# Kernel tuning notes

Measured on AMD Instinct MI355X. Metric: run time of the kernel, lower is better.

The kernel has to match this reference:

```python
import jax, jax.numpy as jnp
import numpy as np

N_NODES = 50000
N_EDGES = 1600000
IN_F = 256
OUT_F = 128
ALPHA = 0.2  # LeakyReLU negative slope
EPS = 1e-9


def setup_inputs() -> dict:
    key = jax.random.key(0)
    k1, k2, k3, k4 = jax.random.split(key, 4)
    x = jax.random.normal(k1, (N_NODES, IN_F), dtype=jnp.float32)
    edge_index = jax.random.randint(k2, (2, N_EDGES), 0, N_NODES, dtype=jnp.int64)
    # xavier_uniform-ish scale for params
    W = jax.random.normal(k3, (IN_F, OUT_F), dtype=jnp.float32) * (1.414 / np.sqrt(IN_F + OUT_F))
    a = jax.random.normal(k4, (1, 2 * OUT_F), dtype=jnp.float32) * (1.414 / np.sqrt(1 + 2 * OUT_F))
    return {"x": x, "edge_index": edge_index, "W": W, "a": a}


def reference(x, edge_index, W, a):
    N = x.shape[0]
    F = W.shape[1]
    h = x @ W                                  # [N, F]
    src = edge_index[0]                        # row indices (aggregation target)
    dst = edge_index[1]                        # col indices (neighbor source)
    a_src = a[0, :F]                           # split a.mm(cat(h_src, h_dst).T)
    a_dst = a[0, F:]
    score = h[src] @ a_src + h[dst] @ a_dst    # [E]
    e = jnp.exp(-jax.nn.leaky_relu(score, negative_slope=ALPHA))  # [E]
    # e_rowsum = A @ ones : sum of edge values per row
    rowsum = jax.ops.segment_sum(e, src, num_segments=N)          # [N]
    # h_prime = A @ h : weighted neighbor aggregation per row
    agg = jax.ops.segment_sum(e[:, None] * h[dst], src, num_segments=N)  # [N, F]
    h_prime = agg / (rowsum[:, None] + EPS)
    return jax.nn.elu(h_prime)  # concat=True -> elu
```

## Files before the change

kernel.cpp:

```cpp
#include <hip/hip_runtime.h>
#include <hip/hip_bf16.h>
#include <math.h>

#define N_NODES 50000
#define N_EDGES 1600000
#define IN_F 256
#define OUT_F 128
#define ALPHA 0.2f
#define EPS 1e-9f

#define NPB 32
#define BINS 1563
#define SUBCAP 1536
#define MAXDEG 128

#define PTILE2 4096
#define PBLKS ((N_EDGES + PTILE2 - 1) / PTILE2)

#define GROWS 32
#define GBLKS ((N_NODES + GROWS - 1) / GROWS)
#define XPITCH 264

typedef __attribute__((ext_vector_type(8))) short short8v;
typedef __attribute__((ext_vector_type(4))) float f32x4;

__device__ __forceinline__ unsigned short bf16r(float f) {
  unsigned u = __float_as_uint(f);
  u = (u + 0x7FFFu + ((u >> 16) & 1u)) >> 16;
  return (unsigned short)u;
}

__device__ __forceinline__ unsigned pk2(float a, float b) {
  unsigned ua = (__float_as_uint(a) + 0x8000u) >> 16;
  unsigned ub = (__float_as_uint(b) + 0x8000u) & 0xFFFF0000u;
  return ua | ub;
}

__global__ __launch_bounds__(256) void wcvt_k(const float* __restrict__ W,
                                              unsigned short* __restrict__ Bf) {
  int fid = blockIdx.x * 256 + threadIdx.x;
  int lane = fid & 63;
  int ks = (fid >> 6) & 7;
  int cg = (fid >> 9) & 1;
  int wv = fid >> 10;
  int col = wv * 32 + cg * 16 + (lane & 15);
  int k0 = ks * 32 + (lane >> 4) * 8;
  unsigned short v[8];
#pragma unroll
  for (int j = 0; j < 8; ++j)
    v[j] = bf16r(W[(size_t)(k0 + j) * OUT_F + col]);
  *reinterpret_cast<short8v*>(&Bf[(size_t)fid * 8]) = *reinterpret_cast<short8v*>(v);
}

__device__ __forceinline__ int load_idx(const int* __restrict__ ei32, int isI64,
                                        long long pos) {
  if (isI64) return (int)(reinterpret_cast<const long long*>(ei32)[pos]);
  return ei32[pos];
}

union SMemU {
  struct {
    unsigned short xsb[GROWS][XPITCH];
    float s1p[GROWS], s2p[GROWS];
  } g;
  struct {
    int hist[BINS], cur[BINS], gbase[BINS];
    int sf64;
  } p;
};

__global__ __launch_bounds__(256) void fused_k(const float* __restrict__ x,
                                               const unsigned short* __restrict__ Bf,
                                               const float* __restrict__ a,
                                               unsigned short* __restrict__ hbs,
                                               float* __restrict__ s1,
                                               float* __restrict__ s2,
                                               const int* __restrict__ ei,
                                               unsigned* __restrict__ bins,
                                               int* __restrict__ bincur) {
  __shared__ SMemU sm;
  const int t = threadIdx.x;

  if (blockIdx.x < PBLKS) {
    if (t < 64) {
      int nz = 0;
#pragma unroll
      for (int j = 0; j < 4; ++j) nz |= ei[2 * (t + j * 64) + 1];
      unsigned long long any = __ballot(nz != 0);
      if (t == 0) sm.p.sf64 = (any == 0ull) ? 1 : 0;
    }
    for (int i = t; i < BINS; i += 256) sm.p.hist[i] = 0;
    __syncthreads();
    const int f64 = sm.p.sf64;
    const int base = blockIdx.x * PTILE2;
    unsigned rec[16];
#pragma unroll
    for (int j = 0; j < 16; ++j) {
      int e = base + j * 256 + t;
      if (e < N_EDGES) {
        unsigned s = (unsigned)load_idx(ei, f64, e);
        unsigned d = (unsigned)load_idx(ei, f64, (long long)N_EDGES + e);
        rec[j] = (s << 16) | d;
        atomicAdd(&sm.p.hist[s >> 5], 1);
      } else rec[j] = 0xFFFFFFFFu;
    }
    __syncthreads();
    for (int i = t; i < BINS; i += 256) {
      sm.p.gbase[i] = sm.p.hist[i] ? atomicAdd(&bincur[i], sm.p.hist[i]) : 0;
      sm.p.cur[i] = 0;
    }
    __syncthreads();
#pragma unroll
    for (int j = 0; j < 16; ++j) {
      if (rec[j] != 0xFFFFFFFFu) {
        int bb = rec[j] >> 21;
        int pos = atomicAdd(&sm.p.cur[bb], 1);
        int o = sm.p.gbase[bb] + pos;
        if (o < SUBCAP) bins[(size_t)bb * SUBCAP + o] = rec[j];
      }
    }
    return;
  }

  const int gbid = blockIdx.x - PBLKS;
  const int lane = t & 63;
  const int wv = t >> 6;
  const int row0 = gbid * GROWS;
  const int wcol0 = wv * 32;
  const int lrow = lane & 15;
  const int hi = lane >> 4;
  const int lk = hi * 8;

  if (t < GROWS) { sm.g.s1p[t] = 0.f; sm.g.s2p[t] = 0.f; }

#pragma unroll
  for (int it = 0; it < 8; ++it) {
    int f4 = it * 256 + t;
    int row = f4 >> 6;
    int c4 = (f4 & 63) * 4;
    int gr = row0 + row;
    if (gr >= N_NODES) gr = N_NODES - 1;
    float4 u = *reinterpret_cast<const float4*>(&x[(size_t)gr * IN_F + c4]);
    unsigned* p = reinterpret_cast<unsigned*>(&sm.g.xsb[row][c4]);
    p[0] = pk2(u.x, u.y);
    p[1] = pk2(u.z, u.w);
  }

  short8v b[2][8];
#pragma unroll
  for (int cg = 0; cg < 2; ++cg)
#pragma unroll
    for (int ks = 0; ks < 8; ++ks)
      b[cg][ks] = *reinterpret_cast<const short8v*>(
          &Bf[(size_t)(((wv * 2 + cg) * 8 + ks) * 64 + lane) * 8]);

  float4 a1v = *reinterpret_cast<const float4*>(&a[wcol0 + 4 * hi]);
  float4 a1w = *reinterpret_cast<const float4*>(&a[wcol0 + 16 + 4 * hi]);
  float4 a2v = *reinterpret_cast<const float4*>(&a[128 + wcol0 + 4 * hi]);
  float4 a2w = *reinterpret_cast<const float4*>(&a[128 + wcol0 + 16 + 4 * hi]);
  __syncthreads();

#pragma unroll
  for (int rg = 0; rg < GROWS / 16; ++rg) {
    short8v av[8];
#pragma unroll
    for (int ks = 0; ks < 8; ++ks)
      av[ks] = *reinterpret_cast<const short8v*>(&sm.g.xsb[rg * 16 + lrow][ks * 32 + lk]);
    f32x4 acc0 = {0.f, 0.f, 0.f, 0.f};
    f32x4 acc1 = {0.f, 0.f, 0.f, 0.f};
#pragma unroll
    for (int ks = 0; ks < 8; ++ks) {
      acc0 = __builtin_amdgcn_mfma_f32_16x16x32_bf16(b[0][ks], av[ks], acc0, 0, 0, 0);
      acc1 = __builtin_amdgcn_mfma_f32_16x16x32_bf16(b[1][ks], av[ks], acc1, 0, 0, 0);
    }
    int xrow = row0 + rg * 16 + lrow;
    if (xrow < N_NODES) {
      uint2 o0 = {pk2(acc0[0], acc0[1]), pk2(acc0[2], acc0[3])};
      uint2 o1 = {pk2(acc1[0], acc1[1]), pk2(acc1[2], acc1[3])};
      *reinterpret_cast<uint2*>(&hbs[(size_t)xrow * OUT_F + wcol0 + 4 * hi]) = o0;
      *reinterpret_cast<uint2*>(&hbs[(size_t)xrow * OUT_F + wcol0 + 16 + 4 * hi]) = o1;
    }
    float p1 = acc0[0] * a1v.x + acc0[1] * a1v.y + acc0[2] * a1v.z + acc0[3] * a1v.w
             + acc1[0] * a1w.x + acc1[1] * a1w.y + acc1[2] * a1w.z + acc1[3] * a1w.w;
    float p2 = acc0[0] * a2v.x + acc0[1] * a2v.y + acc0[2] * a2v.z + acc0[3] * a2v.w
             + acc1[0] * a2w.x + acc1[1] * a2w.y + acc1[2] * a2w.z + acc1[3] * a2w.w;
    p1 += __shfl_xor(p1, 16, 64);
    p2 += __shfl_xor(p2, 16, 64);
    p1 += __shfl_xor(p1, 32, 64);
    p2 += __shfl_xor(p2, 32, 64);
    if (hi == 0) {
      atomicAdd(&sm.g.s1p[rg * 16 + lrow], p1);
      atomicAdd(&sm.g.s2p[rg * 16 + lrow], p2);
    }
  }
  __syncthreads();
  if (t < GROWS) {
    int g = row0 + t;
    if (g < N_NODES) { s1[g] = sm.g.s1p[t]; s2[g] = sm.g.s2p[t]; }
  }
}

__global__ __launch_bounds__(512) void aggc_k(const unsigned* __restrict__ bins,
                                              const int* __restrict__ bincur,
                                              const float* __restrict__ s1,
                                              const float* __restrict__ s2,
                                              const unsigned* __restrict__ hb,
                                              float* __restrict__ out) {
  __shared__ unsigned short sorted[SUBCAP];
  __shared__ uint2 ebuf[8][MAXDEG];
  __shared__ int hist[NPB], cur[NPB], rowptr[NPB + 1];
  const int t = threadIdx.x;
  const int b = blockIdx.x;
  const int lo = b * NPB;
  const int n_b = min(bincur[b], SUBCAP);
  const unsigned* bp = bins + (size_t)b * SUBCAP;

  if (t < NPB) hist[t] = 0;
  __syncthreads();
  unsigned rec[3];
#pragma unroll
  for (int r = 0; r < 3; ++r) {
    int i = t + r * 512;
    rec[r] = 0xFFFFFFFFu;
    if (i < n_b) {
      rec[r] = bp[i];
      atomicAdd(&hist[(rec[r] >> 16) & (NPB - 1)], 1);
    }
  }
  __syncthreads();
  if (t < NPB) {
    int c = hist[t];
    int incl = c;
#pragma unroll
    for (int off = 1; off < NPB; off <<= 1) {
      int v = __shfl_up(incl, off, 64);
      if (t >= off) incl += v;
    }
    rowptr[t + 1] = incl;
    cur[t] = incl - c;
    if (t == 0) rowptr[0] = 0;
  }
  __syncthreads();
#pragma unroll
  for (int r = 0; r < 3; ++r) {
    if (rec[r] != 0xFFFFFFFFu) {
      int sl = (rec[r] >> 16) & (NPB - 1);
      int pos = atomicAdd(&cur[sl], 1);
      sorted[pos] = (unsigned short)(rec[r] & 0xFFFFu);
    }
  }
  __syncthreads();

  const int wv = t >> 6, lane = t & 63;
  for (int i = 0; i < 4; ++i) {
    int nl = wv * 4 + i;
    int g = lo + nl;
    if (g >= N_NODES) continue;
    int rp = rowptr[nl];
    int cn = min(rowptr[nl + 1] - rp, MAXDEG);
    float s1u = s1[g];
    float rsl = 0.f;
    for (int j = lane; j < cn; j += 64) {
      unsigned d = sorted[rp + j];
      float sc = s1u + s2[d];
      float w = __expf(-fmaxf(sc, ALPHA * sc));
      ebuf[wv][j] = make_uint2(d << 6, __float_as_uint(w));
      rsl += w;
    }
#pragma unroll
    for (int m = 32; m >= 1; m >>= 1) rsl += __shfl_xor(rsl, m, 64);
    float accx = 0.f, accy = 0.f;
    int j = 0;
    for (; j + 7 < cn; j += 8) {
      uint4 e0 = *reinterpret_cast<const uint4*>(&ebuf[wv][j]);
      uint4 e1 = *reinterpret_cast<const uint4*>(&ebuf[wv][j + 2]);
      uint4 e2 = *reinterpret_cast<const uint4*>(&ebuf[wv][j + 4]);
      uint4 e3 = *reinterpret_cast<const uint4*>(&ebuf[wv][j + 6]);
      unsigned v0 = hb[e0.x | lane];
      unsigned v1 = hb[e0.z | lane];
      unsigned v2 = hb[e1.x | lane];
      unsigned v3 = hb[e1.z | lane];
      unsigned v4 = hb[e2.x | lane];
      unsigned v5 = hb[e2.z | lane];
      unsigned v6 = hb[e3.x | lane];
      unsigned v7 = hb[e3.z | lane];
      float w0 = __uint_as_float(e0.y), w1 = __uint_as_float(e0.w);
      float w2 = __uint_as_float(e1.y), w3 = __uint_as_float(e1.w);
      float w4 = __uint_as_float(e2.y), w5 = __uint_as_float(e2.w);
      float w6 = __uint_as_float(e3.y), w7 = __uint_as_float(e3.w);
      accx = fmaf(w0, __uint_as_float(v0 << 16), accx);
      accy = fmaf(w0, __uint_as_float(v0 & 0xFFFF0000u), accy);
      accx = fmaf(w1, __uint_as_float(v1 << 16), accx);
      accy = fmaf(w1, __uint_as_float(v1 & 0xFFFF0000u), accy);
      accx = fmaf(w2, __uint_as_float(v2 << 16), accx);
      accy = fmaf(w2, __uint_as_float(v2 & 0xFFFF0000u), accy);
      accx = fmaf(w3, __uint_as_float(v3 << 16), accx);
      accy = fmaf(w3, __uint_as_float(v3 & 0xFFFF0000u), accy);
      accx = fmaf(w4, __uint_as_float(v4 << 16), accx);
      accy = fmaf(w4, __uint_as_float(v4 & 0xFFFF0000u), accy);
      accx = fmaf(w5, __uint_as_float(v5 << 16), accx);
      accy = fmaf(w5, __uint_as_float(v5 & 0xFFFF0000u), accy);
      accx = fmaf(w6, __uint_as_float(v6 << 16), accx);
      accy = fmaf(w6, __uint_as_float(v6 & 0xFFFF0000u), accy);
      accx = fmaf(w7, __uint_as_float(v7 << 16), accx);
      accy = fmaf(w7, __uint_as_float(v7 & 0xFFFF0000u), accy);
    }
    for (; j < cn; ++j) {
      uint2 e = ebuf[wv][j];
      unsigned v0 = hb[e.x | lane];
      float w0 = __uint_as_float(e.y);
      accx = fmaf(w0, __uint_as_float(v0 << 16), accx);
      accy = fmaf(w0, __uint_as_float(v0 & 0xFFFF0000u), accy);
    }
    float inv = 1.0f / (rsl + EPS);
    float px = accx * inv, py = accy * inv;
    px = px > 0.f ? px : expm1f(px);
    py = py > 0.f ? py : expm1f(py);
    float2 o = {px, py};
    *reinterpret_cast<float2*>(&out[(size_t)g * OUT_F + 2 * lane]) = o;
  }
}

extern "C" void kernel_launch(void* const* d_in, const int* in_sizes, int n_in,
                              void* d_out, int out_size, void* d_ws, size_t ws_size,
                              hipStream_t stream) {
  const float* x = (const float*)d_in[0];
  const int* ei = (const int*)d_in[1];
  const float* W = (const float*)d_in[2];
  const float* a = (const float*)d_in[3];
  float* out = (float*)d_out;

  unsigned* hb = (unsigned*)d_ws;
  float* s1 = (float*)(hb + (size_t)N_NODES * 64);
  float* s2 = s1 + N_NODES;
  int* bincur = (int*)(s2 + N_NODES);
  unsigned* bins = (unsigned*)(bincur + BINS);
  unsigned short* Bf = (unsigned short*)(bins + (size_t)BINS * SUBCAP);

  hipMemsetAsync(bincur, 0, (size_t)BINS * sizeof(int), stream);

  wcvt_k<<<16, 256, 0, stream>>>(W, Bf);
  fused_k<<<PBLKS + GBLKS, 256, 0, stream>>>(x, Bf, a, (unsigned short*)hb,
                                             s1, s2, ei, bins, bincur);
  aggc_k<<<BINS, 512, 0, stream>>>(bins, bincur, s1, s2, hb, out);
}
```

Before: 104.0 us.

## Process two row tiles per GEMM block with prefetch of second x tile

Each GEMM block of the fused kernel now covers 64 rows as two 32-row tiles. The second tile's x data is loaded into registers while the first tile's MFMAs run, then packed into a second LDS buffer. This halves the number of GEMM blocks, reuses the per-block B-fragment and attention-vector loads across twice as many rows, and overlaps global loads with compute. The cost is more registers and LDS per block and fewer blocks to spread across CUs.

```diff
diff --git a/kernel.cpp b/kernel.cpp
--- a/kernel.cpp
+++ b/kernel.cpp
@@ -18,7 +18,8 @@
 #define PBLKS ((N_EDGES + PTILE2 - 1) / PTILE2)
 
 #define GROWS 32
-#define GBLKS ((N_NODES + GROWS - 1) / GROWS)
+#define TROWS 64
+#define GBLKS ((N_NODES + TROWS - 1) / TROWS)
 #define XPITCH 264
 
 typedef __attribute__((ext_vector_type(8))) short short8v;
@@ -60,8 +61,8 @@
 
 union SMemU {
   struct {
-    unsigned short xsb[GROWS][XPITCH];
-    float s1p[GROWS], s2p[GROWS];
+    unsigned short xsb[2][GROWS][XPITCH];
+    float s1p[TROWS], s2p[TROWS];
   } g;
   struct {
     int hist[BINS], cur[BINS], gbase[BINS];
@@ -125,13 +126,14 @@
   const int gbid = blockIdx.x - PBLKS;
   const int lane = t & 63;
   const int wv = t >> 6;
-  const int row0 = gbid * GROWS;
+  const int row0 = gbid * TROWS;
   const int wcol0 = wv * 32;
   const int lrow = lane & 15;
   const int hi = lane >> 4;
   const int lk = hi * 8;
-
-  if (t < GROWS) { sm.g.s1p[t] = 0.f; sm.g.s2p[t] = 0.f; }
+  const int srow = (t >> 6);
+
+  if (t < TROWS) { sm.g.s1p[t] = 0.f; sm.g.s2p[t] = 0.f; }
 
 #pragma unroll
   for (int it = 0; it < 8; ++it) {
@@ -141,9 +143,21 @@
     int gr = row0 + row;
     if (gr >= N_NODES) gr = N_NODES - 1;
     float4 u = *reinterpret_cast<const float4*>(&x[(size_t)gr * IN_F + c4]);
-    unsigned* p = reinterpret_cast<unsigned*>(&sm.g.xsb[row][c4]);
+    unsigned* p = reinterpret_cast<unsigned*>(&sm.g.xsb[0][row][c4]);
     p[0] = pk2(u.x, u.y);
     p[1] = pk2(u.z, u.w);
+  }
+  __syncthreads();
+
+  float4 r1[8];
+#pragma unroll
+  for (int it = 0; it < 8; ++it) {
+    int f4 = it * 256 + t;
+    int row = f4 >> 6;
+    int c4 = (f4 & 63) * 4;
+    int gr = row0 + GROWS + row;
+    if (gr >= N_NODES) gr = N_NODES - 1;
+    r1[it] = *reinterpret_cast<const float4*>(&x[(size_t)gr * IN_F + c4]);
   }
 
   short8v b[2][8];
@@ -158,43 +172,58 @@
   float4 a1w = *reinterpret_cast<const float4*>(&a[wcol0 + 16 + 4 * hi]);
   float4 a2v = *reinterpret_cast<const float4*>(&a[128 + wcol0 + 4 * hi]);
   float4 a2w = *reinterpret_cast<const float4*>(&a[128 + wcol0 + 16 + 4 * hi]);
-  __syncthreads();
-
-#pragma unroll
-  for (int rg = 0; rg < GROWS / 16; ++rg) {
-    short8v av[8];
-#pragma unroll
-    for (int ks = 0; ks < 8; ++ks)
-      av[ks] = *reinterpret_cast<const short8v*>(&sm.g.xsb[rg * 16 + lrow][ks * 32 + lk]);
-    f32x4 acc0 = {0.f, 0.f, 0.f, 0.f};
-    f32x4 acc1 = {0.f, 0.f, 0.f, 0.f};
-#pragma unroll
-    for (int ks = 0; ks < 8; ++ks) {
-      acc0 = __builtin_amdgcn_mfma_f32_16x16x32_bf16(b[0][ks], av[ks], acc0, 0, 0, 0);
-      acc1 = __builtin_amdgcn_mfma_f32_16x16x32_bf16(b[1][ks], av[ks], acc1, 0, 0, 0);
-    }
-    int xrow = row0 + rg * 16 + lrow;
-    if (xrow < N_NODES) {
-      uint2 o0 = {pk2(acc0[0], acc0[1]), pk2(acc0[2], acc0[3])};
-      uint2 o1 = {pk2(acc1[0], acc1[1]), pk2(acc1[2], acc1[3])};
-      *reinterpret_cast<uint2*>(&hbs[(size_t)xrow * OUT_F + wcol0 + 4 * hi]) = o0;
-      *reinterpret_cast<uint2*>(&hbs[(size_t)xrow * OUT_F + wcol0 + 16 + 4 * hi]) = o1;
-    }
-    float p1 = acc0[0] * a1v.x + acc0[1] * a1v.y + acc0[2] * a1v.z + acc0[3] * a1v.w
-             + acc1[0] * a1w.x + acc1[1] * a1w.y + acc1[2] * a1w.z + acc1[3] * a1w.w;
-    float p2 = acc0[0] * a2v.x + acc0[1] * a2v.y + acc0[2] * a2v.z + acc0[3] * a2v.w
-             + acc1[0] * a2w.x + acc1[1] * a2w.y + acc1[2] * a2w.z + acc1[3] * a2w.w;
-    p1 += __shfl_xor(p1, 16, 64);
-    p2 += __shfl_xor(p2, 16, 64);
-    p1 += __shfl_xor(p1, 32, 64);
-    p2 += __shfl_xor(p2, 32, 64);
-    if (hi == 0) {
-      atomicAdd(&sm.g.s1p[rg * 16 + lrow], p1);
-      atomicAdd(&sm.g.s2p[rg * 16 + lrow], p2);
-    }
-  }
-  __syncthreads();
-  if (t < GROWS) {
+
+#pragma unroll
+  for (int tile = 0; tile < 2; ++tile) {
+    if (tile == 1) {
+#pragma unroll
+      for (int it = 0; it < 8; ++it) {
+        int f4 = it * 256 + t;
+        int row = f4 >> 6;
+        int c4 = (f4 & 63) * 4;
+        unsigned* p = reinterpret_cast<unsigned*>(&sm.g.xsb[1][row][c4]);
+        p[0] = pk2(r1[it].x, r1[it].y);
+        p[1] = pk2(r1[it].z, r1[it].w);
+      }
+      __syncthreads();
+    }
+#pragma unroll
+    for (int rg = 0; rg < GROWS / 16; ++rg) {
+      short8v av[8];
+#pragma unroll
+      for (int ks = 0; ks < 8; ++ks)
+        av[ks] = *reinterpret_cast<const short8v*>(&sm.g.xsb[tile][rg * 16 + lrow][ks * 32 + lk]);
+      f32x4 acc0 = {0.f, 0.f, 0.f, 0.f};
+      f32x4 acc1 = {0.f, 0.f, 0.f, 0.f};
+#pragma unroll
+      for (int ks = 0; ks < 8; ++ks) {
+        acc0 = __builtin_amdgcn_mfma_f32_16x16x32_bf16(b[0][ks], av[ks], acc0, 0, 0, 0);
+        acc1 = __builtin_amdgcn_mfma_f32_16x16x32_bf16(b[1][ks], av[ks], acc1, 0, 0, 0);
+      }
+      int lr = tile * GROWS + rg * 16 + lrow;
+      int xrow = row0 + lr;
+      if (xrow < N_NODES) {
+        uint2 o0 = {pk2(acc0[0], acc0[1]), pk2(acc0[2], acc0[3])};
+        uint2 o1 = {pk2(acc1[0], acc1[1]), pk2(acc1[2], acc1[3])};
+        *reinterpret_cast<uint2*>(&hbs[(size_t)xrow * OUT_F + wcol0 + 4 * hi]) = o0;
+        *reinterpret_cast<uint2*>(&hbs[(size_t)xrow * OUT_F + wcol0 + 16 + 4 * hi]) = o1;
+      }
+      float p1 = acc0[0] * a1v.x + acc0[1] * a1v.y + acc0[2] * a1v.z + acc0[3] * a1v.w
+               + acc1[0] * a1w.x + acc1[1] * a1w.y + acc1[2] * a1w.z + acc1[3] * a1w.w;
+      float p2 = acc0[0] * a2v.x + acc0[1] * a2v.y + acc0[2] * a2v.z + acc0[3] * a2v.w
+               + acc1[0] * a2w.x + acc1[1] * a2w.y + acc1[2] * a2w.z + acc1[3] * a2w.w;
+      p1 += __shfl_xor(p1, 16, 64);
+      p2 += __shfl_xor(p2, 16, 64);
+      p1 += __shfl_xor(p1, 32, 64);
+      p2 += __shfl_xor(p2, 32, 64);
+      if (hi == 0) {
+        atomicAdd(&sm.g.s1p[lr], p1);
+        atomicAdd(&sm.g.s2p[lr], p2);
+      }
+    }
+  }
+  __syncthreads();
+  if (t < TROWS) {
     int g = row0 + t;
     if (g < N_NODES) { s1[g] = sm.g.s1p[t]; s2[g] = sm.g.s2p[t]; }
   }
```

Result: no change. 103.5 us (-0.4%).
